# Optimization experiments

Hardware: AMD Instinct MI355X
Metric: run time of the kernel (lower is better)

Reference implementation:

```python
import jax, jax.numpy as jnp
import numpy as np

N, E, C, D, H = 50000, 1600000, 50000, 128, 512


def setup_inputs() -> dict:
    key = jax.random.key(0)
    ks = jax.random.split(key, 16)
    s = jnp.float32(0.02)  # keep activations stable through 3 layers
    inp = {}
    inp["x"] = jax.random.normal(ks[0], (N, D), jnp.float32)
    inp["edge_index"] = jax.random.randint(ks[1], (2, E), 0, N)
    inp["first_edge"] = jax.random.randint(ks[2], (2,), 0, N)
    inp["candidate_edges"] = jax.random.randint(ks[3], (C, 2), 0, N)
    inp["t"] = jax.random.uniform(ks[4], (1, 1), jnp.float32)
    dims = [(D, H), (H, H), (H, H)]
    i = 5
    for l, (di, do) in enumerate(dims):
        inp[f"gin{l}_w1"] = jax.random.normal(ks[i], (di, do), jnp.float32) * s; i += 1
        inp[f"gin{l}_b1"] = jnp.zeros((do,), jnp.float32)
        inp[f"gin{l}_w2"] = jax.random.normal(ks[i], (do, do), jnp.float32) * s; i += 1
        inp[f"gin{l}_b2"] = jnp.zeros((do,), jnp.float32)
    inp["pred_w1"] = jax.random.normal(ks[i], (5 * H, H), jnp.float32) * s; i += 1
    inp["pred_b1"] = jnp.zeros((H,), jnp.float32)
    inp["pred_w2"] = jax.random.normal(ks[i], (H, 1), jnp.float32) * s; i += 1
    inp["pred_b2"] = jnp.zeros((1,), jnp.float32)
    inp["time_w1"] = jax.random.normal(ks[i], (1, H), jnp.float32) * s; i += 1
    inp["time_b1"] = jnp.zeros((H,), jnp.float32)
    inp["time_w2"] = jax.random.normal(ks[i], (H, H), jnp.float32) * s; i += 1
    inp["time_b2"] = jnp.zeros((H,), jnp.float32)
    return inp


def _edge_rep(x, u, v):
    # 'sum_absdiff': cat([x_u + x_v, |x_u - x_v|]) -> 2*H features
    xu, xv = x[u], x[v]
    return jnp.concatenate([xu + xv, jnp.abs(xu - xv)], axis=-1)


def reference(x, edge_index, first_edge, candidate_edges, t,
              gin0_w1, gin0_b1, gin0_w2, gin0_b2,
              gin1_w1, gin1_b1, gin1_w2, gin1_b2,
              gin2_w1, gin2_b1, gin2_w2, gin2_b2,
              pred_w1, pred_b1, pred_w2, pred_b2,
              time_w1, time_b1, time_w2, time_b2):
    src, dst = edge_index[0], edge_index[1]
    layers = [(gin0_w1, gin0_b1, gin0_w2, gin0_b2),
              (gin1_w1, gin1_b1, gin1_w2, gin1_b2),
              (gin2_w1, gin2_b1, gin2_w2, gin2_b2)]
    # GINConv (eps=0): h_i = MLP(x_i + sum_{j->i} x_j)
    for w1, b1, w2, b2 in layers:
        agg = jax.ops.segment_sum(x[src], dst, num_segments=x.shape[0])
        h = x + agg
        x = jax.nn.relu(h @ w1 + b1) @ w2 + b2
    first_feat = _edge_rep(x, first_edge[0], first_edge[1])  # [2H]
    t_embed = (jax.nn.relu(t @ time_w1 + time_b1) @ time_w2 + time_b2)[0]  # [H]
    cand_feat = _edge_rep(x, candidate_edges[:, 0], candidate_edges[:, 1])  # [C, 2H]
    Cn = cand_feat.shape[0]
    feat = jnp.concatenate([
        jnp.broadcast_to(first_feat, (Cn, first_feat.shape[0])),
        cand_feat,
        jnp.broadcast_to(t_embed, (Cn, t_embed.shape[0])),
    ], axis=-1)  # [C, 5H]
    logits = (jax.nn.relu(feat @ pred_w1 + pred_b1) @ pred_w2 + pred_b2)[:, 0]  # [C]
    return logits
```

## Files before the change

kernel.cpp:

```cpp
#include <hip/hip_runtime.h>

typedef __bf16 bf16x2 __attribute__((ext_vector_type(2)));
typedef __bf16 bf16x4 __attribute__((ext_vector_type(4)));
typedef __bf16 bf16x8 __attribute__((ext_vector_type(8)));
typedef float f32x4 __attribute__((ext_vector_type(4)));

#define CSR_CHUNKS 256

__device__ __forceinline__ void gload16(const __bf16* g, __bf16* l) {
    __builtin_amdgcn_global_load_lds((const __attribute__((address_space(1))) void*)g,
                                     (__attribute__((address_space(3))) void*)l, 16, 0, 0);
}

__global__ __launch_bounds__(256)
void hist_part_kernel(const int* __restrict__ dst, int* __restrict__ deg, int E, int N) {
    const int r = blockIdx.x & 7;
    const int chunk = blockIdx.x >> 3;
    const int RS = (N + 7) >> 3;
    const int lo = r * RS;
    const int hi = min(lo + RS, N);
    const int stride = CSR_CHUNKS * 256;
    for (int i = chunk * 256 + threadIdx.x; i < E; i += stride) {
        int d = dst[i];
        if (d >= lo && d < hi) atomicAdd(&deg[d], 1);
    }
}

__global__ __launch_bounds__(256)
void scatter_part_kernel(const int* __restrict__ src, const int* __restrict__ dst,
                         int* __restrict__ cursor, int* __restrict__ colsrc, int E, int N) {
    const int r = blockIdx.x & 7;
    const int chunk = blockIdx.x >> 3;
    const int RS = (N + 7) >> 3;
    const int lo = r * RS;
    const int hi = min(lo + RS, N);
    const int stride = CSR_CHUNKS * 256;
    for (int i = chunk * 256 + threadIdx.x; i < E; i += stride) {
        int d = dst[i];
        if (d >= lo && d < hi) {
            int p = atomicAdd(&cursor[d], 1);
            colsrc[p] = src[i];
        }
    }
}

__global__ __launch_bounds__(256)
void blocksum_kernel(const int* __restrict__ deg, int* __restrict__ bsum, int n) {
    __shared__ int red[256];
    int i = blockIdx.x * 256 + threadIdx.x;
    red[threadIdx.x] = (i < n) ? deg[i] : 0;
    __syncthreads();
    for (int off = 128; off > 0; off >>= 1) {
        if (threadIdx.x < off) red[threadIdx.x] += red[threadIdx.x + off];
        __syncthreads();
    }
    if (threadIdx.x == 0) bsum[blockIdx.x] = red[0];
}

__global__ __launch_bounds__(256)
void scanb_kernel(int* __restrict__ bsum, int nb) {
    __shared__ int s[256];
    int t = threadIdx.x;
    s[t] = (t < nb) ? bsum[t] : 0;
    __syncthreads();
    for (int off = 1; off < 256; off <<= 1) {
        int v = (t >= off) ? s[t - off] : 0;
        __syncthreads();
        s[t] += v;
        __syncthreads();
    }
    if (t < nb) bsum[t] = (t == 0) ? 0 : s[t - 1];
}

__global__ __launch_bounds__(256)
void scanw_kernel(const int* __restrict__ deg, const int* __restrict__ bsum,
                  int* __restrict__ rowptr, int* __restrict__ cursor, int n) {
    __shared__ int s[256];
    int b = blockIdx.x, t = threadIdx.x;
    int i = b * 256 + t;
    int d = (i < n) ? deg[i] : 0;
    s[t] = d;
    __syncthreads();
    for (int off = 1; off < 256; off <<= 1) {
        int v = (t >= off) ? s[t - off] : 0;
        __syncthreads();
        s[t] += v;
        __syncthreads();
    }
    int incl = s[t];
    int base = bsum[b];
    if (i < n) {
        int r = base + incl - d;
        rowptr[i] = r;
        cursor[i] = r;
        if (i == n - 1) rowptr[n] = base + incl;
    }
}

__global__ void f32_to_bf16_kernel(const float* __restrict__ in, __bf16* __restrict__ out, int n4) {
    int i = blockIdx.x * 256 + threadIdx.x;
    if (i < n4) {
        float4 f = ((const float4*)in)[i];
        bf16x4 o;
        o[0] = (__bf16)f.x; o[1] = (__bf16)f.y; o[2] = (__bf16)f.z; o[3] = (__bf16)f.w;
        ((bf16x4*)out)[i] = o;
    }
}

__global__ void wprep_kernel(const float* __restrict__ in, __bf16* __restrict__ out, int kbits) {
    int idx = blockIdx.x * 256 + threadIdx.x;
    int K = 1 << kbits;
    if (idx < (512 << kbits)) {
        int k = idx & (K - 1);
        int n = idx >> kbits;
        out[idx] = (__bf16)in[k * 512 + n];
    }
}

template<int F> struct VecT;
template<> struct VecT<2> { using T = bf16x2; };
template<> struct VecT<4> { using T = bf16x4; };
template<> struct VecT<8> { using T = bf16x8; };

template<int F, int U, int STR>
__global__ __launch_bounds__(256)
void agg_kernel(const __bf16* __restrict__ xb, const int* __restrict__ rowptr,
                const int* __restrict__ colsrc, __bf16* __restrict__ h, int n, int colbase) {
    const int node = blockIdx.x * 4 + (threadIdx.x >> 6);
    if (node >= n) return;
    const int lane = threadIdx.x & 63;
    using V = typename VecT<F>::T;

    const __bf16* xl = xb + colbase + lane * F;

    float acc[F];
    {
        V v = *(const V*)(xl + (size_t)node * STR);
        #pragma unroll
        for (int i = 0; i < F; i++) acc[i] = (float)v[i];
    }

    int e   = __builtin_amdgcn_readfirstlane(rowptr[node]);
    int end = __builtin_amdgcn_readfirstlane(rowptr[node + 1]);

    for (; e + U <= end; e += U) {
        int s[U];
        #pragma unroll
        for (int j = 0; j < U; j++) s[j] = colsrc[e + j];
        V v[U];
        #pragma unroll
        for (int j = 0; j < U; j++) v[j] = *(const V*)(xl + (size_t)s[j] * STR);
        #pragma unroll
        for (int j = 0; j < U; j++)
            #pragma unroll
            for (int i = 0; i < F; i++) acc[i] += (float)v[j][i];
    }
    if constexpr (U > 4) {
        for (; e + 4 <= end; e += 4) {
            int s[4];
            #pragma unroll
            for (int j = 0; j < 4; j++) s[j] = colsrc[e + j];
            V v[4];
            #pragma unroll
            for (int j = 0; j < 4; j++) v[j] = *(const V*)(xl + (size_t)s[j] * STR);
            #pragma unroll
            for (int j = 0; j < 4; j++)
                #pragma unroll
                for (int i = 0; i < F; i++) acc[i] += (float)v[j][i];
        }
    }
    for (; e < end; e++) {
        int s0 = colsrc[e];
        V v = *(const V*)(xl + (size_t)s0 * STR);
        #pragma unroll
        for (int i = 0; i < F; i++) acc[i] += (float)v[i];
    }

    __bf16* out = h + colbase + (size_t)node * STR + lane * F;
    V o;
    #pragma unroll
    for (int i = 0; i < F; i++) o[i] = (__bf16)acc[i];
    *(V*)out = o;
}

template<int AMODE, bool RELU>
__global__ __launch_bounds__(256, 3)
void gemm_kernel(const __bf16* __restrict__ A, const __bf16* __restrict__ Xb,
                 const int* __restrict__ cand, const __bf16* __restrict__ Bt,
                 const float* __restrict__ bias, __bf16* __restrict__ Cout,
                 int M, int K) {
    __shared__ __bf16 smem[2 * (2048 + 8192)];
    __bf16* const sA0 = smem;
    __bf16* const sA1 = smem + 2048;
    __bf16* const sB0 = smem + 4096;
    __bf16* const sB1 = smem + 4096 + 8192;

    const int bx = blockIdx.x;
    const int rblk = (bx >> 4) * 8 + (bx & 7);
    const int panel = (bx >> 3) & 1;
    const int rowBase = rblk * 64;
    if (rowBase >= M) return;
    const int nBase = panel * 256;

    const int tid = threadIdx.x;
    const int lane = tid & 63;
    const int wid = tid >> 6;
    const int mlane = lane & 15;
    const int quad = lane >> 4;

    const int swzc = (((lane & 3) ^ ((lane >> 3) & 3)) << 3);

    const int aRow = rowBase + wid * 16 + (lane >> 2);
    const int aRowC = (aRow < M) ? aRow : (M - 1);
    const __bf16* aSrc = A + (size_t)aRowC * K + swzc;
    const int bRow = nBase + wid * 64 + (lane >> 2);
    const __bf16* bSrc = Bt + (size_t)bRow * K + swzc;

    const int rkey = (mlane >> 1) & 3;
    const int base_r = mlane * 32 + ((quad ^ rkey) << 3);

    const int ar = tid >> 2;
    const int acn = tid & 3;
    const int ac = acn << 3;
    const int wkey = (ar >> 1) & 3;
    const int woffA = ar * 32 + ((acn ^ wkey) << 3);

    f32x4 acc[4][4];
    #pragma unroll
    for (int i = 0; i < 4; i++)
        #pragma unroll
        for (int j = 0; j < 4; j++) acc[i][j] = f32x4{0.f, 0.f, 0.f, 0.f};

    int uu = 0, vv = 0;
    const int grow = rowBase + ar;
    const bool arowok = (grow < M);
    if (AMODE == 1 && arowok) { uu = cand[2 * grow]; vv = cand[2 * grow + 1]; }

    bf16x8 pxu{}, pxv{};
    int pk = 0;

    auto stageB = [&](__bf16* bufB, int k0) {
        #pragma unroll
        for (int j = 0; j < 4; j++)
            gload16(bSrc + (size_t)j * 16 * K + k0, bufB + wid * 2048 + j * 512);
    };
    auto stageA0 = [&](__bf16* bufA, int k0) {
        gload16(aSrc + k0, bufA + wid * 512);
    };
    auto issueA1 = [&](int k0) {
        pk = k0;
        if (arowok) {
            int kk = (k0 + ac) & 511;
            pxu = *(const bf16x8*)(Xb + (size_t)uu * 512 + kk);
            pxv = *(const bf16x8*)(Xb + (size_t)vv * 512 + kk);
        }
    };
    auto commitA1 = [&](__bf16* bufA) {
        bf16x8 av = bf16x8{};
        if (arowok) {
            if (pk + ac < 512) {
                #pragma unroll
                for (int q = 0; q < 8; q++) av[q] = (__bf16)((float)pxu[q] + (float)pxv[q]);
            } else {
                #pragma unroll
                for (int q = 0; q < 8; q++) av[q] = (__bf16)fabsf((float)pxu[q] - (float)pxv[q]);
            }
        }
        *(bf16x8*)(bufA + woffA) = av;
    };

    auto compute = [&](const __bf16* bufA, const __bf16* bufB) {
        bf16x8 aF[4], bF[4];
        #pragma unroll
        for (int mt = 0; mt < 4; mt++)
            aF[mt] = *(const bf16x8*)(bufA + mt * 512 + base_r);
        #pragma unroll
        for (int nt = 0; nt < 4; nt++)
            bF[nt] = *(const bf16x8*)(bufB + wid * 2048 + nt * 512 + base_r);
        #pragma unroll
        for (int mt = 0; mt < 4; mt++)
            #pragma unroll
            for (int nt = 0; nt < 4; nt++)
                acc[mt][nt] = __builtin_amdgcn_mfma_f32_16x16x32_bf16(aF[mt], bF[nt], acc[mt][nt], 0, 0, 0);
    };

    const int nt = K >> 5;
    if (AMODE == 0) {
        stageA0(sA0, 0);
        stageB(sB0, 0);
        __builtin_amdgcn_sched_barrier(0);
        stageA0(sA1, 32);
        stageB(sB1, 32);
        asm volatile("s_waitcnt vmcnt(5)" ::: "memory");
        __builtin_amdgcn_s_barrier();
        __builtin_amdgcn_sched_barrier(0);

        int cur = 0;
        for (int t = 0; t < nt; ++t) {
            __bf16* cA = cur ? sA1 : sA0;
            __bf16* cB = cur ? sB1 : sB0;
            compute(cA, cB);
            if (t + 1 < nt) {
                __builtin_amdgcn_s_barrier();
                __builtin_amdgcn_sched_barrier(0);
                if (t + 2 < nt) {
                    stageA0(cA, (t + 2) << 5);
                    stageB(cB, (t + 2) << 5);
                    asm volatile("s_waitcnt vmcnt(5)" ::: "memory");
                } else {
                    asm volatile("s_waitcnt vmcnt(0)" ::: "memory");
                }
                __builtin_amdgcn_s_barrier();
                __builtin_amdgcn_sched_barrier(0);
                cur ^= 1;
            }
        }
    } else {
        issueA1(0);
        commitA1(sA0);
        stageB(sB0, 0);
        __syncthreads();
        for (int t = 0; t < nt; t += 2) {
            issueA1((t + 1) << 5);
            stageB(sB1, (t + 1) << 5);
            compute(sA0, sB0);
            commitA1(sA1);
            __syncthreads();
            if (t + 2 < nt) {
                issueA1((t + 2) << 5);
                stageB(sB0, (t + 2) << 5);
            }
            compute(sA1, sB1);
            if (t + 2 < nt) commitA1(sA0);
            __syncthreads();
        }
    }

    float bv[4];
    #pragma unroll
    for (int nt2 = 0; nt2 < 4; nt2++) bv[nt2] = bias[nBase + wid * 64 + nt2 * 16 + mlane];

    float* tp = (float*)smem;
    const int erow = tid >> 4;
    const int ecg = tid & 15;
    #pragma unroll
    for (int mt = 0; mt < 4; mt++) {
        __syncthreads();
        #pragma unroll
        for (int nt2 = 0; nt2 < 4; nt2++) {
            #pragma unroll
            for (int r = 0; r < 4; r++) {
                float v = acc[mt][nt2][r] + bv[nt2];
                if (RELU) v = fmaxf(v, 0.f);
                tp[(quad * 4 + r) * 260 + wid * 64 + nt2 * 16 + mlane] = v;
            }
        }
        __syncthreads();
        int gr = rowBase + mt * 16 + erow;
        if (gr < M) {
            const float* rp = tp + erow * 260 + ecg * 16;
            f32x4 a = *(const f32x4*)(rp);
            f32x4 b = *(const f32x4*)(rp + 4);
            f32x4 c = *(const f32x4*)(rp + 8);
            f32x4 d = *(const f32x4*)(rp + 12);
            bf16x8 o0, o1;
            #pragma unroll
            for (int j = 0; j < 4; j++) { o0[j] = (__bf16)a[j]; o0[4 + j] = (__bf16)b[j]; }
            #pragma unroll
            for (int j = 0; j < 4; j++) { o1[j] = (__bf16)c[j]; o1[4 + j] = (__bf16)d[j]; }
            __bf16* op = Cout + (size_t)gr * 512 + nBase + ecg * 16;
            *(bf16x8*)op = o0;
            *(bf16x8*)(op + 8) = o1;
        }
    }
}

__global__ __launch_bounds__(512)
void constvec_kernel(const __bf16* __restrict__ xb, const int* __restrict__ first_edge,
                     const float* __restrict__ t,
                     const float* __restrict__ tw1, const float* __restrict__ tb1,
                     const float* __restrict__ tw2, const float* __restrict__ tb2,
                     const float* __restrict__ pw1, const float* __restrict__ pb1,
                     float* __restrict__ cvec) {
    __shared__ float z1[512];
    __shared__ float te[512];
    __shared__ float ff[1024];
    int tid = threadIdx.x;
    float tv = t[0];
    z1[tid] = fmaxf(tv * tw1[tid] + tb1[tid], 0.f);
    int u = first_edge[0], v = first_edge[1];
    float xu = (float)xb[(size_t)u * 512 + tid];
    float xv = (float)xb[(size_t)v * 512 + tid];
    ff[tid] = xu + xv;
    ff[512 + tid] = fabsf(xu - xv);
    __syncthreads();
    float s = tb2[tid];
    for (int j = 0; j < 512; j++) s += z1[j] * tw2[j * 512 + tid];
    te[tid] = s;
    __syncthreads();
    float c = pb1[tid];
    for (int k = 0; k < 1024; k++) c += ff[k] * pw1[k * 512 + tid];
    for (int j = 0; j < 512; j++) c += te[j] * pw1[(2048 + j) * 512 + tid];
    cvec[tid] = c;
}

__global__ __launch_bounds__(256)
void logits_kernel(const __bf16* __restrict__ Z, const float* __restrict__ w2,
                   const float* __restrict__ b2, float* __restrict__ out, int C) {
    int c = blockIdx.x * 4 + (threadIdx.x >> 6);
    if (c >= C) return;
    int lane = threadIdx.x & 63;
    bf16x8 z = *(const bf16x8*)(Z + (size_t)c * 512 + lane * 8);
    const float4* w = (const float4*)(w2 + lane * 8);
    float4 w0 = w[0], w1 = w[1];
    float s = (float)z[0] * w0.x + (float)z[1] * w0.y + (float)z[2] * w0.z + (float)z[3] * w0.w
            + (float)z[4] * w1.x + (float)z[5] * w1.y + (float)z[6] * w1.z + (float)z[7] * w1.w;
    #pragma unroll
    for (int off = 32; off > 0; off >>= 1) s += __shfl_down(s, off);
    if (lane == 0) out[c] = s + b2[0];
}

extern "C" void kernel_launch(void* const* d_in, const int* in_sizes, int n_in,
                              void* d_out, int out_size, void* d_ws, size_t ws_size,
                              hipStream_t stream) {
    (void)n_in; (void)out_size; (void)ws_size;
    const float* x          = (const float*)d_in[0];
    const int*   edge_index = (const int*)d_in[1];
    const int*   first_edge = (const int*)d_in[2];
    const int*   cand       = (const int*)d_in[3];
    const float* t          = (const float*)d_in[4];
    const float* gw1[3] = {(const float*)d_in[5], (const float*)d_in[9],  (const float*)d_in[13]};
    const float* gb1[3] = {(const float*)d_in[6], (const float*)d_in[10], (const float*)d_in[14]};
    const float* gw2[3] = {(const float*)d_in[7], (const float*)d_in[11], (const float*)d_in[15]};
    const float* gb2[3] = {(const float*)d_in[8], (const float*)d_in[12], (const float*)d_in[16]};
    const float* pw1 = (const float*)d_in[17];
    const float* pb1 = (const float*)d_in[18];
    const float* pw2 = (const float*)d_in[19];
    const float* pb2 = (const float*)d_in[20];
    const float* tw1 = (const float*)d_in[21];
    const float* tb1 = (const float*)d_in[22];
    const float* tw2 = (const float*)d_in[23];
    const float* tb2 = (const float*)d_in[24];

    const int N = in_sizes[0] / 128;
    const int E = in_sizes[1] / 2;
    const int C = in_sizes[3] / 2;

    char* p = (char*)d_ws;
    auto alloc = [&](size_t bytes) -> void* {
        void* r = (void*)p;
        p += (bytes + 255) & ~(size_t)255;
        return r;
    };
    __bf16* h    = (__bf16*)alloc((size_t)N * 512 * 2);
    __bf16* u    = (__bf16*)alloc((size_t)N * 512 * 2);
    __bf16* xb   = (__bf16*)alloc((size_t)N * 512 * 2);
    __bf16* wt01 = (__bf16*)alloc((size_t)512 * 128 * 2);
    __bf16* wt02 = (__bf16*)alloc((size_t)512 * 512 * 2);
    __bf16* wt11 = (__bf16*)alloc((size_t)512 * 512 * 2);
    __bf16* wt12 = (__bf16*)alloc((size_t)512 * 512 * 2);
    __bf16* wt21 = (__bf16*)alloc((size_t)512 * 512 * 2);
    __bf16* wt22 = (__bf16*)alloc((size_t)512 * 512 * 2);
    __bf16* wtH  = (__bf16*)alloc((size_t)512 * 1024 * 2);
    int* rowptr = (int*)alloc((size_t)(N + 1) * 4);
    int* deg    = (int*)alloc((size_t)N * 4);
    int* cursor = (int*)alloc((size_t)N * 4);
    int* colsrc = (int*)alloc((size_t)E * 4);
    int* bsum   = (int*)alloc((size_t)256 * 4);
    float* cvec = (float*)alloc(512 * 4);
    __bf16* xb0 = (__bf16*)u;

    const int* src = edge_index;
    const int* dst = edge_index + E;

    hipMemsetAsync(deg, 0, (size_t)N * 4, stream);
    int nb = (N + 255) / 256;
    hist_part_kernel<<<CSR_CHUNKS * 8, 256, 0, stream>>>(dst, deg, E, N);
    blocksum_kernel<<<nb, 256, 0, stream>>>(deg, bsum, N);
    scanb_kernel<<<1, 256, 0, stream>>>(bsum, nb);
    scanw_kernel<<<nb, 256, 0, stream>>>(deg, bsum, rowptr, cursor, N);
    scatter_part_kernel<<<CSR_CHUNKS * 8, 256, 0, stream>>>(src, dst, cursor, colsrc, E, N);

    f32_to_bf16_kernel<<<((N * 128 / 4) + 255) / 256, 256, 0, stream>>>(x, xb0, N * 128 / 4);
    wprep_kernel<<<((512 << 7)  + 255) / 256, 256, 0, stream>>>(gw1[0], wt01, 7);
    wprep_kernel<<<((512 << 9)  + 255) / 256, 256, 0, stream>>>(gw2[0], wt02, 9);
    wprep_kernel<<<((512 << 9)  + 255) / 256, 256, 0, stream>>>(gw1[1], wt11, 9);
    wprep_kernel<<<((512 << 9)  + 255) / 256, 256, 0, stream>>>(gw2[1], wt12, 9);
    wprep_kernel<<<((512 << 9)  + 255) / 256, 256, 0, stream>>>(gw1[2], wt21, 9);
    wprep_kernel<<<((512 << 9)  + 255) / 256, 256, 0, stream>>>(gw2[2], wt22, 9);
    wprep_kernel<<<((512 << 10) + 255) / 256, 256, 0, stream>>>(pw1 + (size_t)1024 * 512, wtH, 10);

    const int Rblk = (N + 63) / 64;
    const int gpair = ((Rblk + 7) / 8) * 16;
    int ablocks = (N + 3) / 4;

    agg_kernel<2, 16, 128><<<ablocks, 256, 0, stream>>>(xb0, rowptr, colsrc, h, N, 0);
    gemm_kernel<0, true ><<<gpair, 256, 0, stream>>>(h, nullptr, nullptr, wt01, gb1[0], u,  N, 128);
    gemm_kernel<0, false><<<gpair, 256, 0, stream>>>(u, nullptr, nullptr, wt02, gb2[0], xb, N, 512);
    agg_kernel<4, 8, 512><<<ablocks, 256, 0, stream>>>(xb, rowptr, colsrc, h, N, 0);
    agg_kernel<4, 8, 512><<<ablocks, 256, 0, stream>>>(xb, rowptr, colsrc, h, N, 256);
    gemm_kernel<0, true ><<<gpair, 256, 0, stream>>>(h, nullptr, nullptr, wt11, gb1[1], u,  N, 512);
    gemm_kernel<0, false><<<gpair, 256, 0, stream>>>(u, nullptr, nullptr, wt12, gb2[1], xb, N, 512);
    agg_kernel<4, 8, 512><<<ablocks, 256, 0, stream>>>(xb, rowptr, colsrc, h, N, 0);
    agg_kernel<4, 8, 512><<<ablocks, 256, 0, stream>>>(xb, rowptr, colsrc, h, N, 256);
    gemm_kernel<0, true ><<<gpair, 256, 0, stream>>>(h, nullptr, nullptr, wt21, gb1[2], u,  N, 512);
    gemm_kernel<0, false><<<gpair, 256, 0, stream>>>(u, nullptr, nullptr, wt22, gb2[2], xb, N, 512);

    constvec_kernel<<<1, 512, 0, stream>>>(xb, first_edge, t, tw1, tb1, tw2, tb2, pw1, pb1, cvec);
    gemm_kernel<1, true><<<gpair, 256, 0, stream>>>(nullptr, xb, cand, wtH, cvec, u, C, 1024);
    logits_kernel<<<(C + 3) / 4, 256, 0, stream>>>(u, pw2, pb2, (float*)d_out, C);
}
```

Before: 1.193 ms.

## Compute full 512-column output per block in node GEMMs with 512-thread tiles

Adds a gemmF kernel where each 512-thread block computes a 64x512 output tile (8 waves, each covering 64 columns), so the A tile is loaded once per row block instead of once per 256-column panel. The six GIN-layer GEMMs now use it, and the old gemm kernel keeps only the candidate-gather path. The aim is to halve A-operand global traffic and the number of blocks. In exchange it uses about 72KB of LDS with launch_bounds(512,1), which lowers occupancy and may hurt latency hiding.

Result: slower. 1.227 ms (+2.9%).

```diff
diff --git a/kernel.cpp b/kernel.cpp
--- a/kernel.cpp
+++ b/kernel.cpp
@@ -183,6 +183,135 @@
     *(V*)out = o;
 }
 
+template<bool RELU>
+__global__ __launch_bounds__(512, 1)
+void gemmF_kernel(const __bf16* __restrict__ A, const __bf16* __restrict__ Bt,
+                  const float* __restrict__ bias, __bf16* __restrict__ Cout,
+                  int M, int K) {
+    __shared__ __bf16 smem[36864];
+    __bf16* const sA0 = smem;
+    __bf16* const sA1 = smem + 2048;
+    __bf16* const sB0 = smem + 4096;
+    __bf16* const sB1 = smem + 20480;
+
+    const int tid = threadIdx.x;
+    const int lane = tid & 63;
+    const int wid = tid >> 6;
+    const int mlane = lane & 15;
+    const int quad = lane >> 4;
+    const int rowBase = blockIdx.x * 64;
+
+    const int swzc = (((lane & 3) ^ ((lane >> 3) & 3)) << 3);
+
+    const int aRow = rowBase + wid * 16 + (lane >> 2);
+    const int aRowC = (aRow < M) ? aRow : (M - 1);
+    const __bf16* aSrc = A + (size_t)aRowC * K + swzc;
+    const int bRow = wid * 64 + (lane >> 2);
+    const __bf16* bSrc = Bt + (size_t)bRow * K + swzc;
+
+    const int rkey = (mlane >> 1) & 3;
+    const int base_r = mlane * 32 + ((quad ^ rkey) << 3);
+
+    f32x4 acc[4][4];
+    #pragma unroll
+    for (int i = 0; i < 4; i++)
+        #pragma unroll
+        for (int j = 0; j < 4; j++) acc[i][j] = f32x4{0.f, 0.f, 0.f, 0.f};
+
+    auto stage = [&](__bf16* bufA, __bf16* bufB, int k0) {
+        if (wid < 4) gload16(aSrc + k0, bufA + wid * 512);
+        #pragma unroll
+        for (int j = 0; j < 4; j++)
+            gload16(bSrc + (size_t)j * 16 * K + k0, bufB + wid * 2048 + j * 512);
+    };
+    auto waitc = [&]() {
+        if (wid < 4) { asm volatile("s_waitcnt vmcnt(5)" ::: "memory"); }
+        else         { asm volatile("s_waitcnt vmcnt(4)" ::: "memory"); }
+    };
+    auto compute = [&](const __bf16* bufA, const __bf16* bufB) {
+        bf16x8 aF[4], bF[4];
+        #pragma unroll
+        for (int mt = 0; mt < 4; mt++)
+            aF[mt] = *(const bf16x8*)(bufA + mt * 512 + base_r);
+        #pragma unroll
+        for (int nt = 0; nt < 4; nt++)
+            bF[nt] = *(const bf16x8*)(bufB + wid * 2048 + nt * 512 + base_r);
+        #pragma unroll
+        for (int mt = 0; mt < 4; mt++)
+            #pragma unroll
+            for (int nt = 0; nt < 4; nt++)
+                acc[mt][nt] = __builtin_amdgcn_mfma_f32_16x16x32_bf16(aF[mt], bF[nt], acc[mt][nt], 0, 0, 0);
+    };
+
+    const int nt = K >> 5;
+    stage(sA0, sB0, 0);
+    __builtin_amdgcn_sched_barrier(0);
+    stage(sA1, sB1, 32);
+    waitc();
+    __builtin_amdgcn_sched_barrier(0);
+    __builtin_amdgcn_s_barrier();
+    __builtin_amdgcn_sched_barrier(0);
+
+    int cur = 0;
+    for (int t = 0; t < nt; ++t) {
+        __bf16* cA = cur ? sA1 : sA0;
+        __bf16* cB = cur ? sB1 : sB0;
+        compute(cA, cB);
+        if (t + 1 < nt) {
+            __builtin_amdgcn_s_barrier();
+            __builtin_amdgcn_sched_barrier(0);
+            if (t + 2 < nt) {
+                stage(cA, cB, (t + 2) << 5);
+                waitc();
+            } else {
+                asm volatile("s_waitcnt vmcnt(0)" ::: "memory");
+            }
+            __builtin_amdgcn_sched_barrier(0);
+            __builtin_amdgcn_s_barrier();
+            __builtin_amdgcn_sched_barrier(0);
+            cur ^= 1;
+        }
+    }
+
+    float bv[4];
+    #pragma unroll
+    for (int nt2 = 0; nt2 < 4; nt2++) bv[nt2] = bias[wid * 64 + nt2 * 16 + mlane];
+
+    float* tp = (float*)smem;
+    const int erow = tid >> 5;
+    const int ecg = tid & 31;
+    #pragma unroll
+    for (int mt = 0; mt < 4; mt++) {
+        __syncthreads();
+        #pragma unroll
+        for (int nt2 = 0; nt2 < 4; nt2++) {
+            #pragma unroll
+            for (int r = 0; r < 4; r++) {
+                float v = acc[mt][nt2][r] + bv[nt2];
+                if (RELU) v = fmaxf(v, 0.f);
+                tp[(quad * 4 + r) * 520 + wid * 64 + nt2 * 16 + mlane] = v;
+            }
+        }
+        __syncthreads();
+        int gr = rowBase + mt * 16 + erow;
+        if (gr < M) {
+            const float* rp = tp + erow * 520 + ecg * 16;
+            f32x4 a = *(const f32x4*)(rp);
+            f32x4 b = *(const f32x4*)(rp + 4);
+            f32x4 c = *(const f32x4*)(rp + 8);
+            f32x4 d = *(const f32x4*)(rp + 12);
+            bf16x8 o0, o1;
+            #pragma unroll
+            for (int j = 0; j < 4; j++) { o0[j] = (__bf16)a[j]; o0[4 + j] = (__bf16)b[j]; }
+            #pragma unroll
+            for (int j = 0; j < 4; j++) { o1[j] = (__bf16)c[j]; o1[4 + j] = (__bf16)d[j]; }
+            __bf16* op = Cout + (size_t)gr * 512 + ecg * 16;
+            *(bf16x8*)op = o0;
+            *(bf16x8*)(op + 8) = o1;
+        }
+    }
+}
+
 template<int AMODE, bool RELU>
 __global__ __launch_bounds__(256, 3)
 void gemm_kernel(const __bf16* __restrict__ A, const __bf16* __restrict__ Xb,
@@ -209,10 +338,6 @@
     const int quad = lane >> 4;
 
     const int swzc = (((lane & 3) ^ ((lane >> 3) & 3)) << 3);
-
-    const int aRow = rowBase + wid * 16 + (lane >> 2);
-    const int aRowC = (aRow < M) ? aRow : (M - 1);
-    const __bf16* aSrc = A + (size_t)aRowC * K + swzc;
     const int bRow = nBase + wid * 64 + (lane >> 2);
     const __bf16* bSrc = Bt + (size_t)bRow * K + swzc;
 
@@ -243,9 +368,6 @@
         #pragma unroll
         for (int j = 0; j < 4; j++)
             gload16(bSrc + (size_t)j * 16 * K + k0, bufB + wid * 2048 + j * 512);
-    };
-    auto stageA0 = [&](__bf16* bufA, int k0) {
-        gload16(aSrc + k0, bufA + wid * 512);
     };
     auto issueA1 = [&](int k0) {
         pk = k0;
@@ -285,55 +407,23 @@
     };
 
     const int nt = K >> 5;
-    if (AMODE == 0) {
-        stageA0(sA0, 0);
-        stageB(sB0, 0);
-        __builtin_amdgcn_sched_barrier(0);
-        stageA0(sA1, 32);
-        stageB(sB1, 32);
-        asm volatile("s_waitcnt vmcnt(5)" ::: "memory");
-        __builtin_amdgcn_s_barrier();
-        __builtin_amdgcn_sched_barrier(0);
-
-        int cur = 0;
-        for (int t = 0; t < nt; ++t) {
-            __bf16* cA = cur ? sA1 : sA0;
-            __bf16* cB = cur ? sB1 : sB0;
-            compute(cA, cB);
-            if (t + 1 < nt) {
-                __builtin_amdgcn_s_barrier();
-                __builtin_amdgcn_sched_barrier(0);
-                if (t + 2 < nt) {
-                    stageA0(cA, (t + 2) << 5);
-                    stageB(cB, (t + 2) << 5);
-                    asm volatile("s_waitcnt vmcnt(5)" ::: "memory");
-                } else {
-                    asm volatile("s_waitcnt vmcnt(0)" ::: "memory");
-                }
-                __builtin_amdgcn_s_barrier();
-                __builtin_amdgcn_sched_barrier(0);
-                cur ^= 1;
-            }
-        }
-    } else {
-        issueA1(0);
-        commitA1(sA0);
-        stageB(sB0, 0);
-        __syncthreads();
-        for (int t = 0; t < nt; t += 2) {
-            issueA1((t + 1) << 5);
-            stageB(sB1, (t + 1) << 5);
-            compute(sA0, sB0);
-            commitA1(sA1);
-            __syncthreads();
-            if (t + 2 < nt) {
-                issueA1((t + 2) << 5);
-                stageB(sB0, (t + 2) << 5);
-            }
-            compute(sA1, sB1);
-            if (t + 2 < nt) commitA1(sA0);
-            __syncthreads();
-        }
+    issueA1(0);
+    commitA1(sA0);
+    stageB(sB0, 0);
+    __syncthreads();
+    for (int t = 0; t < nt; t += 2) {
+        issueA1((t + 1) << 5);
+        stageB(sB1, (t + 1) << 5);
+        compute(sA0, sB0);
+        commitA1(sA1);
+        __syncthreads();
+        if (t + 2 < nt) {
+            issueA1((t + 2) << 5);
+            stageB(sB0, (t + 2) << 5);
+        }
+        compute(sA1, sB1);
+        if (t + 2 < nt) commitA1(sA0);
+        __syncthreads();
     }
 
     float bv[4];
@@ -495,16 +585,16 @@
     int ablocks = (N + 3) / 4;
 
     agg_kernel<2, 16, 128><<<ablocks, 256, 0, stream>>>(xb0, rowptr, colsrc, h, N, 0);
-    gemm_kernel<0, true ><<<gpair, 256, 0, stream>>>(h, nullptr, nullptr, wt01, gb1[0], u,  N, 128);
-    gemm_kernel<0, false><<<gpair, 256, 0, stream>>>(u, nullptr, nullptr, wt02, gb2[0], xb, N, 512);
+    gemmF_kernel<true ><<<Rblk, 512, 0, stream>>>(h, wt01, gb1[0], u,  N, 128);
+    gemmF_kernel<false><<<Rblk, 512, 0, stream>>>(u, wt02, gb2[0], xb, N, 512);
     agg_kernel<4, 8, 512><<<ablocks, 256, 0, stream>>>(xb, rowptr, colsrc, h, N, 0);
     agg_kernel<4, 8, 512><<<ablocks, 256, 0, stream>>>(xb, rowptr, colsrc, h, N, 256);
-    gemm_kernel<0, true ><<<gpair, 256, 0, stream>>>(h, nullptr, nullptr, wt11, gb1[1], u,  N, 512);
-    gemm_kernel<0, false><<<gpair, 256, 0, stream>>>(u, nullptr, nullptr, wt12, gb2[1], xb, N, 512);
+    gemmF_kernel<true ><<<Rblk, 512, 0, stream>>>(h, wt11, gb1[1], u,  N, 512);
+    gemmF_kernel<false><<<Rblk, 512, 0, stream>>>(u, wt12, gb2[1], xb, N, 512);
     agg_kernel<4, 8, 512><<<ablocks, 256, 0, stream>>>(xb, rowptr, colsrc, h, N, 0);
     agg_kernel<4, 8, 512><<<ablocks, 256, 0, stream>>>(xb, rowptr, colsrc, h, N, 256);
-    gemm_kernel<0, true ><<<gpair, 256, 0, stream>>>(h, nullptr, nullptr, wt21, gb1[2], u,  N, 512);
-    gemm_kernel<0, false><<<gpair, 256, 0, stream>>>(u, nullptr, nullptr, wt22, gb2[2], xb, N, 512);
+    gemmF_kernel<true ><<<Rblk, 512, 0, stream>>>(h, wt21, gb1[2], u,  N, 512);
+    gemmF_kernel<false><<<Rblk, 512, 0, stream>>>(u, wt22, gb2[2], xb, N, 512);
 
     constvec_kernel<<<1, 512, 0, stream>>>(xb, first_edge, t, tw1, tb1, tw2, tb2, pw1, pb1, cvec);
     gemm_kernel<1, true><<<gpair, 256, 0, stream>>>(nullptr, xb, cand, wtH, cvec, u, C, 1024);
```
